# Kernel tuning notes

Measured on AMD Instinct MI355X. Metric: run time of the kernel, lower is better.

Reference implementation:

```python
import jax, jax.numpy as jnp
import numpy as np

H, W = 256, 256
N = 1024
EPS2D = 1e-4  # regularizer added to 2D covariances before inversion


def setup_inputs() -> dict:
    key = jax.random.key(0)
    ks = jax.random.split(key, 6)
    xy = jax.random.normal(ks[0], (N, 2), dtype=jnp.float32) * 3.0
    z = jax.random.uniform(ks[1], (N, 1), minval=2.0, maxval=30.0, dtype=jnp.float32)
    means3D = jnp.concatenate([xy, z], axis=-1)                      # [N,3], depths in (1,50)
    A = 0.1 * jax.random.normal(ks[2], (N, 3, 3), dtype=jnp.float32)
    covs3d = A @ jnp.swapaxes(A, -1, -2) + 0.01 * jnp.eye(3, dtype=jnp.float32)  # SPD [N,3,3]
    colors = jax.random.uniform(ks[3], (N, 3), dtype=jnp.float32)
    opacities = jax.random.uniform(ks[4], (N,), dtype=jnp.float32)
    Kmat = jnp.array([[300.0, 0.0, W / 2.0], [0.0, 300.0, H / 2.0], [0.0, 0.0, 1.0]], dtype=jnp.float32)
    Rmat = jnp.eye(3, dtype=jnp.float32)
    t = jnp.zeros((3,), dtype=jnp.float32)
    return {"means3D": means3D, "covs3d": covs3d, "colors": colors,
            "opacities": opacities, "K": Kmat, "R": Rmat, "t": t}


def reference(means3D, covs3d, colors, opacities, K, R, t):
    n = means3D.shape[0]
    # ---- projection ----
    cam = means3D @ R.T + t[None, :]                      # [N,3]
    depths = jnp.maximum(cam[:, 2], 1.0)
    screen = cam @ K.T
    means2D = screen[:, :2] / screen[:, 2:3]              # [N,2]
    fx, fy = K[0, 0], K[1, 1]
    inv_z = 1.0 / cam[:, 2]
    z2 = cam[:, 2] ** 2
    zeros = jnp.zeros_like(inv_z)
    row0 = jnp.stack([inv_z * fx, zeros, -cam[:, 0] / z2 * fx], axis=-1)
    row1 = jnp.stack([zeros, inv_z * fy, -cam[:, 1] / z2 * fy], axis=-1)
    J = jnp.stack([row0, row1], axis=1)                   # [N,2,3]
    covs_cam = jnp.einsum('ij,njk,lk->nil', R, covs3d, R)  # [N,3,3]
    covs2D = jnp.einsum('nij,njk,nlk->nil', J, covs_cam, J)  # [N,2,2]

    # ---- depth sort ----
    order = jnp.argsort(depths)
    means2D = means2D[order]
    covs2D = covs2D[order]
    colors_s = colors[order]
    opac_s = opacities[order]
    depths_s = depths[order]
    valid = (depths_s > 1.0) & (depths_s < 50.0)

    # ---- per-pixel gaussian evaluation (closed-form 2x2 inverse == cholesky_inverse) ----
    covs2D = covs2D + EPS2D * jnp.eye(2, dtype=covs2D.dtype)
    a = covs2D[:, 0, 0]; b = covs2D[:, 0, 1]; c = covs2D[:, 1, 1]
    det = a * c - b * b                                   # [N]
    ia = c / det; ib = -b / det; ic = a / det

    yy, xx = jnp.meshgrid(jnp.arange(H, dtype=jnp.float32),
                          jnp.arange(W, dtype=jnp.float32), indexing='ij')
    dx0 = xx[None] - means2D[:, 0, None, None]            # [N,H,W]
    dx1 = yy[None] - means2D[:, 1, None, None]            # [N,H,W]
    q = (ia[:, None, None] * dx0 * dx0
         + 2.0 * ib[:, None, None] * dx0 * dx1
         + ic[:, None, None] * dx1 * dx1)
    gauss = jnp.exp(-0.5 * q) / (2.0 * jnp.pi * jnp.sqrt(det))[:, None, None]
    gauss = gauss * valid[:, None, None].astype(gauss.dtype)

    # ---- alpha compositing (front-to-back) ----
    alphas = opac_s[:, None, None] * gauss                # [N,H,W]
    T = jnp.cumprod(1.0 - alphas, axis=0)
    T = jnp.concatenate([jnp.ones_like(alphas[:1]), T[:-1]], axis=0)
    weights = T * alphas                                  # [N,H,W]
    rendered = jnp.einsum('nhw,nc->hwc', weights, colors_s)  # [H,W,3]
    return rendered
```

## Files before the change

### kernel.cpp

```cpp
#include <hip/hip_runtime.h>
#include <math.h>

#define HH 256
#define WW 256
#define EPS2D 1e-4f
#define MAXN 1024
#define CULL_THR 23.0f
#define NL_HALF_LOG2E -0.72134752044448170368f


__global__ __launch_bounds__(256) void prep_kernel(
    const float* __restrict__ means3D, const float* __restrict__ covs3d,
    const float* __restrict__ colors,  const float* __restrict__ opac,
    const float* __restrict__ Km,      const float* __restrict__ Rm,
    const float* __restrict__ tv,
    float4* __restrict__ A, float4* __restrict__ B, float* __restrict__ C,
    int n)
{
    __shared__ float s_mean[MAXN*3];
    __shared__ float s_depth[MAXN];
    __shared__ float s_cov[64*9];
    __shared__ float s_col[64*3];
    __shared__ float s_op[64];
    __shared__ int   s_pr[4][64];

    int t = threadIdx.x, lane = t & 63, w = t >> 6;
    int g0b = blockIdx.x * 64;
    int nb = n - g0b; if (nb > 64) nb = 64; if (nb < 0) nb = 0;

    {
        int nm4 = (3*n) >> 2;
        const float4* m4 = (const float4*)means3D;
        for (int i = t; i < nm4; i += 256) ((float4*)s_mean)[i] = m4[i];
        for (int i = (nm4<<2) + t; i < 3*n; i += 256) s_mean[i] = means3D[i];

        const float* cbase = covs3d + (size_t)g0b * 9;
        int ncf = nb * 9, nc4 = ncf >> 2;
        for (int i = t; i < nc4; i += 256) ((float4*)s_cov)[i] = ((const float4*)cbase)[i];
        for (int i = (nc4<<2) + t; i < ncf; i += 256) s_cov[i] = cbase[i];

        const float* lbase = colors + (size_t)g0b * 3;
        int nlf = nb * 3, nl4 = nlf >> 2;
        for (int i = t; i < nl4; i += 256) ((float4*)s_col)[i] = ((const float4*)lbase)[i];
        for (int i = (nl4<<2) + t; i < nlf; i += 256) s_col[i] = lbase[i];

        const float* obase = opac + g0b;
        int no4 = nb >> 2;
        for (int i = t; i < no4; i += 256) ((float4*)s_op)[i] = ((const float4*)obase)[i];
        for (int i = (no4<<2) + t; i < nb; i += 256) s_op[i] = obase[i];
    }
    __syncthreads();

    float R00=Rm[0],R01=Rm[1],R02=Rm[2];
    float R10=Rm[3],R11=Rm[4],R12=Rm[5];
    float R20=Rm[6],R21=Rm[7],R22=Rm[8];
    float t0=tv[0], t1=tv[1], t2=tv[2];

    for (int g = t; g < MAXN; g += 256) {
        float d = 1e30f;
        if (g < n) {
            float X=s_mean[3*g+0], Y=s_mean[3*g+1], Z=s_mean[3*g+2];
            float cz = R20*X + R21*Y + R22*Z + t2;
            d = fmaxf(cz, 1.0f);
        }
        s_depth[g] = d;
    }
    __syncthreads();

    float mx=0.f,my=0.f,qa=0.f,qb=0.f,qc=0.f,lk=0.f,cr=0.f,cg=0.f,cbv=0.f;
    if (w == 0 && lane < nb) {
        int i = g0b + lane;
        float X = s_mean[3*i+0], Y = s_mean[3*i+1], Z = s_mean[3*i+2];
        float cx = R00*X + R01*Y + R02*Z + t0;
        float cy = R10*X + R11*Y + R12*Z + t1;
        float cz = R20*X + R21*Y + R22*Z + t2;
        float depth = s_depth[i];

        float K00=Km[0],K01=Km[1],K02=Km[2];
        float K10=Km[3],K11=Km[4],K12=Km[5];
        float K20=Km[6],K21=Km[7],K22=Km[8];
        float sx = K00*cx + K01*cy + K02*cz;
        float sy = K10*cx + K11*cy + K12*cz;
        float sz = K20*cx + K21*cy + K22*cz;
        mx = sx / sz;
        my = sy / sz;

        float invz  = 1.0f / cz;
        float invz2 = invz * invz;
        float j00 =  K00 * invz;
        float j02 = -K00 * cx * invz2;
        float j11 =  K11 * invz;
        float j12 = -K11 * cy * invz2;

        const float* S = s_cov + 9*lane;
        float S00=S[0],S01=S[1],S02=S[2];
        float S10=S[3],S11=S[4],S12=S[5];
        float S20=S[6],S21=S[7],S22=S[8];

        float M00 = R00*S00 + R01*S10 + R02*S20;
        float M01 = R00*S01 + R01*S11 + R02*S21;
        float M02 = R00*S02 + R01*S12 + R02*S22;
        float M10 = R10*S00 + R11*S10 + R12*S20;
        float M11 = R10*S01 + R11*S11 + R12*S21;
        float M12 = R10*S02 + R11*S12 + R12*S22;
        float M20 = R20*S00 + R21*S10 + R22*S20;
        float M21 = R20*S01 + R21*S11 + R22*S21;
        float M22 = R20*S02 + R21*S12 + R22*S22;
        float C00 = M00*R00 + M01*R01 + M02*R02;
        float C01 = M00*R10 + M01*R11 + M02*R12;
        float C02 = M00*R20 + M01*R21 + M02*R22;
        float C11 = M10*R10 + M11*R11 + M12*R12;
        float C12 = M10*R20 + M11*R21 + M12*R22;
        float C22 = M20*R20 + M21*R21 + M22*R22;

        float a_ = j00*j00*C00 + 2.0f*j00*j02*C02 + j02*j02*C22 + EPS2D;
        float b_ = j00*j11*C01 + j00*j12*C02 + j02*j11*C12 + j02*j12*C22;
        float c_ = j11*j11*C11 + 2.0f*j11*j12*C12 + j12*j12*C22 + EPS2D;

        float det = a_ * c_ - b_ * b_;
        float ia =  c_ / det;
        float ib = -b_ / det;
        float ic =  a_ / det;
        float norm = 1.0f / (6.283185307179586f * sqrtf(det));

        bool valid = (depth > 1.0f) && (depth < 50.0f);
        float k = s_op[lane] * norm * (valid ? 1.0f : 0.0f);

        qa = NL_HALF_LOG2E * ia;
        qb = 2.0f * NL_HALF_LOG2E * ib;
        qc = NL_HALF_LOG2E * ic;
        lk = log2f(k);
        cr = s_col[3*lane+0];
        cg = s_col[3*lane+1];
        cbv = s_col[3*lane+2];
    }

    {
        int cnt = 0;
        if (lane < nb) {
            int i = g0b + lane;
            float d = s_depth[i];
            const float4* d4 = (const float4*)s_depth;
            int jb = w * 64;
            #pragma unroll 4
            for (int jj = 0; jj < 64; ++jj) {
                float4 v = d4[jb + jj];
                int j = (jb + jj) << 2;
                cnt += (v.x < d || (v.x == d && j+0 < i)) ? 1 : 0;
                cnt += (v.y < d || (v.y == d && j+1 < i)) ? 1 : 0;
                cnt += (v.z < d || (v.z == d && j+2 < i)) ? 1 : 0;
                cnt += (v.w < d || (v.w == d && j+3 < i)) ? 1 : 0;
            }
        }
        s_pr[w][lane] = cnt;
    }
    __syncthreads();

    if (w == 0 && lane < nb) {
        int rank = s_pr[0][lane] + s_pr[1][lane] + s_pr[2][lane] + s_pr[3][lane];
        A[rank] = make_float4(mx, my, qa, qb);
        B[rank] = make_float4(qc, lk, cr, cg);
        C[rank] = cbv;
    }
}

__global__ __launch_bounds__(256) void render_kernel(
    const float4* __restrict__ A, const float4* __restrict__ B,
    const float* __restrict__ C, float* __restrict__ out, int n)
{
    __shared__ float4 s_p0[4][256];
    __shared__ float4 s_p1[4][256];
    __shared__ float4 s_part[3][256];

    int t = threadIdx.x, lane = t & 63, w = t >> 6;
    int row = blockIdx.x;
    int q0 = (n *  w     ) >> 2;
    int q1 = (n * (w + 1)) >> 2;
    float pyf = (float)row;

    int cnt = 0;
    if (q1 > q0) {
        int jc = min(q0 + lane, q1 - 1);
        float4 a = A[jc];
        float4 b = B[jc];
        float  c = C[jc];
        for (int ch = q0; ch < q1; ch += 64) {
            float4 a_n, b_n; float c_n;
            int cn = ch + 64;
            if (cn < q1) {
                int jc2 = min(cn + lane, q1 - 1);
                a_n = A[jc2];
                b_n = B[jc2];
                c_n = C[jc2];
            }
            int jj = ch + lane;
            bool keep = false;
            float qbdy = 0.f, u = 0.f;
            if (jj < q1) {
                float dy = pyf - a.y;
                qbdy = a.w * dy;
                u    = fmaf(b.x * dy, dy, b.y);
                float disc = fmaf(qbdy, qbdy, -4.0f * a.z * (u + CULL_THR));
                if (disc > 0.0f) {
                    float inv2qa = 0.5f / a.z;
                    float shw = sqrtf(disc) * inv2qa;
                    float ctr = -qbdy * inv2qa;
                    float xl = a.x + ctr + shw;
                    float xr = a.x + ctr - shw;
                    keep = (xr >= 0.0f) && (xl <= 255.0f);
                }
            }
            unsigned long long mk = __ballot(keep);
            int pre = __popcll(mk & ((1ull << lane) - 1ull));
            if (keep) {
                int pos = cnt + pre;
                s_p0[w][pos] = make_float4(a.x, a.z, qbdy, u);
                s_p1[w][pos] = make_float4(b.z, b.w, c, 0.f);
            }
            cnt += __popcll(mk);
            a = a_n; b = b_n; c = c_n;
        }
    }

    float lanef = (float)lane;
    float T0=1.f,T1=1.f,T2=1.f,T3=1.f;
    float r0=0.f,g0=0.f,b0=0.f, r1=0.f,g1=0.f,b1=0.f;
    float r2=0.f,g2=0.f,b2=0.f, r3=0.f,g3=0.f,b3=0.f;

    for (int k = 0; k < cnt; ++k) {
        float4 p0 = s_p0[w][k];
        float4 p1 = s_p1[w][k];
        float dx = lanef - p0.x;
        {
            float q = fmaf(fmaf(p0.y, dx, p0.z), dx, p0.w);
            float wg = T0 * __builtin_amdgcn_exp2f(q);
            r0 = fmaf(wg, p1.x, r0); g0 = fmaf(wg, p1.y, g0);
            b0 = fmaf(wg, p1.z, b0); T0 -= wg;
        }
        dx += 64.0f;
        {
            float q = fmaf(fmaf(p0.y, dx, p0.z), dx, p0.w);
            float wg = T1 * __builtin_amdgcn_exp2f(q);
            r1 = fmaf(wg, p1.x, r1); g1 = fmaf(wg, p1.y, g1);
            b1 = fmaf(wg, p1.z, b1); T1 -= wg;
        }
        dx += 64.0f;
        {
            float q = fmaf(fmaf(p0.y, dx, p0.z), dx, p0.w);
            float wg = T2 * __builtin_amdgcn_exp2f(q);
            r2 = fmaf(wg, p1.x, r2); g2 = fmaf(wg, p1.y, g2);
            b2 = fmaf(wg, p1.z, b2); T2 -= wg;
        }
        dx += 64.0f;
        {
            float q = fmaf(fmaf(p0.y, dx, p0.z), dx, p0.w);
            float wg = T3 * __builtin_amdgcn_exp2f(q);
            r3 = fmaf(wg, p1.x, r3); g3 = fmaf(wg, p1.y, g3);
            b3 = fmaf(wg, p1.z, b3); T3 -= wg;
        }
    }

    if (w != 0) {
        s_part[w-1][lane +   0] = make_float4(r0, g0, b0, T0);
        s_part[w-1][lane +  64] = make_float4(r1, g1, b1, T1);
        s_part[w-1][lane + 128] = make_float4(r2, g2, b2, T2);
        s_part[w-1][lane + 192] = make_float4(r3, g3, b3, T3);
    }
    __syncthreads();
    if (w == 0) {
        float rr[4]  = {r0, r1, r2, r3};
        float gg[4]  = {g0, g1, g2, g3};
        float bbv[4] = {b0, b1, b2, b3};
        float tt[4]  = {T0, T1, T2, T3};
        #pragma unroll
        for (int i = 0; i < 4; ++i) {
            int px = lane + (i << 6);
            float4 m1 = s_part[0][px];
            float4 m2 = s_part[1][px];
            float4 m3 = s_part[2][px];
            float cr = m2.x + m2.w * m3.x;
            float cg = m2.y + m2.w * m3.y;
            float cb = m2.z + m2.w * m3.z;
            cr = m1.x + m1.w * cr;
            cg = m1.y + m1.w * cg;
            cb = m1.z + m1.w * cb;
            cr = rr[i] + tt[i] * cr;
            cg = gg[i] + tt[i] * cg;
            cb = bbv[i] + tt[i] * cb;
            int p = row * 256 + px;
            out[3*p+0] = cr;
            out[3*p+1] = cg;
            out[3*p+2] = cb;
        }
    }
}

extern "C" void kernel_launch(void* const* d_in, const int* in_sizes, int n_in,
                              void* d_out, int out_size, void* d_ws, size_t ws_size,
                              hipStream_t stream)
{
    const float* means3D = (const float*)d_in[0];
    const float* covs3d  = (const float*)d_in[1];
    const float* colors  = (const float*)d_in[2];
    const float* opac    = (const float*)d_in[3];
    const float* Km      = (const float*)d_in[4];
    const float* Rm      = (const float*)d_in[5];
    const float* tv      = (const float*)d_in[6];
    int n = in_sizes[3];
    if (n > MAXN) n = MAXN;

    float4* A = (float4*)d_ws;
    float4* B = (float4*)((char*)d_ws + 16384);
    float*  C = (float*)((char*)d_ws + 32768);

    int pblocks = (n + 63) / 64;
    hipLaunchKernelGGL(prep_kernel, dim3(pblocks), dim3(256), 0, stream,
                       means3D, covs3d, colors, opac, Km, Rm, tv, A, B, C, n);

    hipLaunchKernelGGL(render_kernel, dim3(HH), dim3(256), 0, stream,
                       A, B, C, (float*)d_out, n);
}
```

Baseline: 23.48 us.

## Fuse prep and render into one cooperative kernel with grid sync

Merges the projection/sort prep kernel and the per-row render kernel into a single cooperative launch. The first few blocks do the prep work, then all 256 blocks meet at a grid-wide barrier before rendering. This removes the second kernel launch and the gap between the two kernels. In exchange it adds a grid sync and makes every block carry the combined shared-memory footprint, which could lower occupancy or make the cooperative launch fail if 256 blocks cannot be co-resident.

```diff
diff --git a/kernel.cpp b/kernel.cpp
--- a/kernel.cpp
+++ b/kernel.cpp
@@ -1,5 +1,8 @@
 #include <hip/hip_runtime.h>
+#include <hip/hip_cooperative_groups.h>
 #include <math.h>
+
+namespace cg = cooperative_groups;
 
 #define HH 256
 #define WW 256
@@ -9,13 +12,13 @@
 #define NL_HALF_LOG2E -0.72134752044448170368f
 
 
-__global__ __launch_bounds__(256) void prep_kernel(
+__global__ __launch_bounds__(256) void fused_kernel(
     const float* __restrict__ means3D, const float* __restrict__ covs3d,
     const float* __restrict__ colors,  const float* __restrict__ opac,
     const float* __restrict__ Km,      const float* __restrict__ Rm,
     const float* __restrict__ tv,
     float4* __restrict__ A, float4* __restrict__ B, float* __restrict__ C,
-    int n)
+    float* __restrict__ out, int n)
 {
     __shared__ float s_mean[MAXN*3];
     __shared__ float s_depth[MAXN];
@@ -23,157 +26,157 @@
     __shared__ float s_col[64*3];
     __shared__ float s_op[64];
     __shared__ int   s_pr[4][64];
-
-    int t = threadIdx.x, lane = t & 63, w = t >> 6;
-    int g0b = blockIdx.x * 64;
-    int nb = n - g0b; if (nb > 64) nb = 64; if (nb < 0) nb = 0;
-
-    {
-        int nm4 = (3*n) >> 2;
-        const float4* m4 = (const float4*)means3D;
-        for (int i = t; i < nm4; i += 256) ((float4*)s_mean)[i] = m4[i];
-        for (int i = (nm4<<2) + t; i < 3*n; i += 256) s_mean[i] = means3D[i];
-
-        const float* cbase = covs3d + (size_t)g0b * 9;
-        int ncf = nb * 9, nc4 = ncf >> 2;
-        for (int i = t; i < nc4; i += 256) ((float4*)s_cov)[i] = ((const float4*)cbase)[i];
-        for (int i = (nc4<<2) + t; i < ncf; i += 256) s_cov[i] = cbase[i];
-
-        const float* lbase = colors + (size_t)g0b * 3;
-        int nlf = nb * 3, nl4 = nlf >> 2;
-        for (int i = t; i < nl4; i += 256) ((float4*)s_col)[i] = ((const float4*)lbase)[i];
-        for (int i = (nl4<<2) + t; i < nlf; i += 256) s_col[i] = lbase[i];
-
-        const float* obase = opac + g0b;
-        int no4 = nb >> 2;
-        for (int i = t; i < no4; i += 256) ((float4*)s_op)[i] = ((const float4*)obase)[i];
-        for (int i = (no4<<2) + t; i < nb; i += 256) s_op[i] = obase[i];
-    }
-    __syncthreads();
-
-    float R00=Rm[0],R01=Rm[1],R02=Rm[2];
-    float R10=Rm[3],R11=Rm[4],R12=Rm[5];
-    float R20=Rm[6],R21=Rm[7],R22=Rm[8];
-    float t0=tv[0], t1=tv[1], t2=tv[2];
-
-    for (int g = t; g < MAXN; g += 256) {
-        float d = 1e30f;
-        if (g < n) {
-            float X=s_mean[3*g+0], Y=s_mean[3*g+1], Z=s_mean[3*g+2];
-            float cz = R20*X + R21*Y + R22*Z + t2;
-            d = fmaxf(cz, 1.0f);
-        }
-        s_depth[g] = d;
-    }
-    __syncthreads();
-
-    float mx=0.f,my=0.f,qa=0.f,qb=0.f,qc=0.f,lk=0.f,cr=0.f,cg=0.f,cbv=0.f;
-    if (w == 0 && lane < nb) {
-        int i = g0b + lane;
-        float X = s_mean[3*i+0], Y = s_mean[3*i+1], Z = s_mean[3*i+2];
-        float cx = R00*X + R01*Y + R02*Z + t0;
-        float cy = R10*X + R11*Y + R12*Z + t1;
-        float cz = R20*X + R21*Y + R22*Z + t2;
-        float depth = s_depth[i];
-
-        float K00=Km[0],K01=Km[1],K02=Km[2];
-        float K10=Km[3],K11=Km[4],K12=Km[5];
-        float K20=Km[6],K21=Km[7],K22=Km[8];
-        float sx = K00*cx + K01*cy + K02*cz;
-        float sy = K10*cx + K11*cy + K12*cz;
-        float sz = K20*cx + K21*cy + K22*cz;
-        mx = sx / sz;
-        my = sy / sz;
-
-        float invz  = 1.0f / cz;
-        float invz2 = invz * invz;
-        float j00 =  K00 * invz;
-        float j02 = -K00 * cx * invz2;
-        float j11 =  K11 * invz;
-        float j12 = -K11 * cy * invz2;
-
-        const float* S = s_cov + 9*lane;
-        float S00=S[0],S01=S[1],S02=S[2];
-        float S10=S[3],S11=S[4],S12=S[5];
-        float S20=S[6],S21=S[7],S22=S[8];
-
-        float M00 = R00*S00 + R01*S10 + R02*S20;
-        float M01 = R00*S01 + R01*S11 + R02*S21;
-        float M02 = R00*S02 + R01*S12 + R02*S22;
-        float M10 = R10*S00 + R11*S10 + R12*S20;
-        float M11 = R10*S01 + R11*S11 + R12*S21;
-        float M12 = R10*S02 + R11*S12 + R12*S22;
-        float M20 = R20*S00 + R21*S10 + R22*S20;
-        float M21 = R20*S01 + R21*S11 + R22*S21;
-        float M22 = R20*S02 + R21*S12 + R22*S22;
-        float C00 = M00*R00 + M01*R01 + M02*R02;
-        float C01 = M00*R10 + M01*R11 + M02*R12;
-        float C02 = M00*R20 + M01*R21 + M02*R22;
-        float C11 = M10*R10 + M11*R11 + M12*R12;
-        float C12 = M10*R20 + M11*R21 + M12*R22;
-        float C22 = M20*R20 + M21*R21 + M22*R22;
-
-        float a_ = j00*j00*C00 + 2.0f*j00*j02*C02 + j02*j02*C22 + EPS2D;
-        float b_ = j00*j11*C01 + j00*j12*C02 + j02*j11*C12 + j02*j12*C22;
-        float c_ = j11*j11*C11 + 2.0f*j11*j12*C12 + j12*j12*C22 + EPS2D;
-
-        float det = a_ * c_ - b_ * b_;
-        float ia =  c_ / det;
-        float ib = -b_ / det;
-        float ic =  a_ / det;
-        float norm = 1.0f / (6.283185307179586f * sqrtf(det));
-
-        bool valid = (depth > 1.0f) && (depth < 50.0f);
-        float k = s_op[lane] * norm * (valid ? 1.0f : 0.0f);
-
-        qa = NL_HALF_LOG2E * ia;
-        qb = 2.0f * NL_HALF_LOG2E * ib;
-        qc = NL_HALF_LOG2E * ic;
-        lk = log2f(k);
-        cr = s_col[3*lane+0];
-        cg = s_col[3*lane+1];
-        cbv = s_col[3*lane+2];
-    }
-
-    {
-        int cnt = 0;
-        if (lane < nb) {
-            int i = g0b + lane;
-            float d = s_depth[i];
-            const float4* d4 = (const float4*)s_depth;
-            int jb = w * 64;
-            #pragma unroll 4
-            for (int jj = 0; jj < 64; ++jj) {
-                float4 v = d4[jb + jj];
-                int j = (jb + jj) << 2;
-                cnt += (v.x < d || (v.x == d && j+0 < i)) ? 1 : 0;
-                cnt += (v.y < d || (v.y == d && j+1 < i)) ? 1 : 0;
-                cnt += (v.z < d || (v.z == d && j+2 < i)) ? 1 : 0;
-                cnt += (v.w < d || (v.w == d && j+3 < i)) ? 1 : 0;
-            }
-        }
-        s_pr[w][lane] = cnt;
-    }
-    __syncthreads();
-
-    if (w == 0 && lane < nb) {
-        int rank = s_pr[0][lane] + s_pr[1][lane] + s_pr[2][lane] + s_pr[3][lane];
-        A[rank] = make_float4(mx, my, qa, qb);
-        B[rank] = make_float4(qc, lk, cr, cg);
-        C[rank] = cbv;
-    }
-}
-
-__global__ __launch_bounds__(256) void render_kernel(
-    const float4* __restrict__ A, const float4* __restrict__ B,
-    const float* __restrict__ C, float* __restrict__ out, int n)
-{
     __shared__ float4 s_p0[4][256];
     __shared__ float4 s_p1[4][256];
     __shared__ float4 s_part[3][256];
 
     int t = threadIdx.x, lane = t & 63, w = t >> 6;
-    int row = blockIdx.x;
+    int blk = blockIdx.x;
+    int pblocks = (n + 63) >> 6;
+
+    if (blk < pblocks) {
+        int g0b = blk * 64;
+        int nb = n - g0b; if (nb > 64) nb = 64;
+
+        {
+            int nm4 = (3*n) >> 2;
+            const float4* m4 = (const float4*)means3D;
+            for (int i = t; i < nm4; i += 256) ((float4*)s_mean)[i] = m4[i];
+            for (int i = (nm4<<2) + t; i < 3*n; i += 256) s_mean[i] = means3D[i];
+
+            const float* cbase = covs3d + (size_t)g0b * 9;
+            int ncf = nb * 9, nc4 = ncf >> 2;
+            for (int i = t; i < nc4; i += 256) ((float4*)s_cov)[i] = ((const float4*)cbase)[i];
+            for (int i = (nc4<<2) + t; i < ncf; i += 256) s_cov[i] = cbase[i];
+
+            const float* lbase = colors + (size_t)g0b * 3;
+            int nlf = nb * 3, nl4 = nlf >> 2;
+            for (int i = t; i < nl4; i += 256) ((float4*)s_col)[i] = ((const float4*)lbase)[i];
+            for (int i = (nl4<<2) + t; i < nlf; i += 256) s_col[i] = lbase[i];
+
+            const float* obase = opac + g0b;
+            int no4 = nb >> 2;
+            for (int i = t; i < no4; i += 256) ((float4*)s_op)[i] = ((const float4*)obase)[i];
+            for (int i = (no4<<2) + t; i < nb; i += 256) s_op[i] = obase[i];
+        }
+        __syncthreads();
+
+        float R00=Rm[0],R01=Rm[1],R02=Rm[2];
+        float R10=Rm[3],R11=Rm[4],R12=Rm[5];
+        float R20=Rm[6],R21=Rm[7],R22=Rm[8];
+        float t0=tv[0], t1=tv[1], t2=tv[2];
+
+        for (int g = t; g < MAXN; g += 256) {
+            float d = 1e30f;
+            if (g < n) {
+                float X=s_mean[3*g+0], Y=s_mean[3*g+1], Z=s_mean[3*g+2];
+                float cz = R20*X + R21*Y + R22*Z + t2;
+                d = fmaxf(cz, 1.0f);
+            }
+            s_depth[g] = d;
+        }
+        __syncthreads();
+
+        float mx=0.f,my=0.f,qa=0.f,qb=0.f,qc=0.f,lk=0.f,cr=0.f,cg_=0.f,cbv=0.f;
+        if (w == 0 && lane < nb) {
+            int i = g0b + lane;
+            float X = s_mean[3*i+0], Y = s_mean[3*i+1], Z = s_mean[3*i+2];
+            float cx = R00*X + R01*Y + R02*Z + t0;
+            float cy = R10*X + R11*Y + R12*Z + t1;
+            float cz = R20*X + R21*Y + R22*Z + t2;
+            float depth = s_depth[i];
+
+            float K00=Km[0],K01=Km[1],K02=Km[2];
+            float K10=Km[3],K11=Km[4],K12=Km[5];
+            float K20=Km[6],K21=Km[7],K22=Km[8];
+            float sx = K00*cx + K01*cy + K02*cz;
+            float sy = K10*cx + K11*cy + K12*cz;
+            float sz = K20*cx + K21*cy + K22*cz;
+            mx = sx / sz;
+            my = sy / sz;
+
+            float invz  = 1.0f / cz;
+            float invz2 = invz * invz;
+            float j00 =  K00 * invz;
+            float j02 = -K00 * cx * invz2;
+            float j11 =  K11 * invz;
+            float j12 = -K11 * cy * invz2;
+
+            const float* S = s_cov + 9*lane;
+            float S00=S[0],S01=S[1],S02=S[2];
+            float S10=S[3],S11=S[4],S12=S[5];
+            float S20=S[6],S21=S[7],S22=S[8];
+
+            float M00 = R00*S00 + R01*S10 + R02*S20;
+            float M01 = R00*S01 + R01*S11 + R02*S21;
+            float M02 = R00*S02 + R01*S12 + R02*S22;
+            float M10 = R10*S00 + R11*S10 + R12*S20;
+            float M11 = R10*S01 + R11*S11 + R12*S21;
+            float M12 = R10*S02 + R11*S12 + R12*S22;
+            float M20 = R20*S00 + R21*S10 + R22*S20;
+            float M21 = R20*S01 + R21*S11 + R22*S21;
+            float M22 = R20*S02 + R21*S12 + R22*S22;
+            float C00 = M00*R00 + M01*R01 + M02*R02;
+            float C01 = M00*R10 + M01*R11 + M02*R12;
+            float C02 = M00*R20 + M01*R21 + M02*R22;
+            float C11 = M10*R10 + M11*R11 + M12*R12;
+            float C12 = M10*R20 + M11*R21 + M12*R22;
+            float C22 = M20*R20 + M21*R21 + M22*R22;
+
+            float a_ = j00*j00*C00 + 2.0f*j00*j02*C02 + j02*j02*C22 + EPS2D;
+            float b_ = j00*j11*C01 + j00*j12*C02 + j02*j11*C12 + j02*j12*C22;
+            float c_ = j11*j11*C11 + 2.0f*j11*j12*C12 + j12*j12*C22 + EPS2D;
+
+            float det = a_ * c_ - b_ * b_;
+            float ia =  c_ / det;
+            float ib = -b_ / det;
+            float ic =  a_ / det;
+            float norm = 1.0f / (6.283185307179586f * sqrtf(det));
+
+            bool valid = (depth > 1.0f) && (depth < 50.0f);
+            float k = s_op[lane] * norm * (valid ? 1.0f : 0.0f);
+
+            qa = NL_HALF_LOG2E * ia;
+            qb = 2.0f * NL_HALF_LOG2E * ib;
+            qc = NL_HALF_LOG2E * ic;
+            lk = log2f(k);
+            cr  = s_col[3*lane+0];
+            cg_ = s_col[3*lane+1];
+            cbv = s_col[3*lane+2];
+        }
+
+        {
+            int cnt = 0;
+            if (lane < nb) {
+                int i = g0b + lane;
+                float d = s_depth[i];
+                const float4* d4 = (const float4*)s_depth;
+                int jb = w * 64;
+                #pragma unroll 4
+                for (int jj = 0; jj < 64; ++jj) {
+                    float4 v = d4[jb + jj];
+                    int j = (jb + jj) << 2;
+                    cnt += (v.x < d || (v.x == d && j+0 < i)) ? 1 : 0;
+                    cnt += (v.y < d || (v.y == d && j+1 < i)) ? 1 : 0;
+                    cnt += (v.z < d || (v.z == d && j+2 < i)) ? 1 : 0;
+                    cnt += (v.w < d || (v.w == d && j+3 < i)) ? 1 : 0;
+                }
+            }
+            s_pr[w][lane] = cnt;
+        }
+        __syncthreads();
+
+        if (w == 0 && lane < nb) {
+            int rank = s_pr[0][lane] + s_pr[1][lane] + s_pr[2][lane] + s_pr[3][lane];
+            A[rank] = make_float4(mx, my, qa, qb);
+            B[rank] = make_float4(qc, lk, cr, cg_);
+            C[rank] = cbv;
+        }
+    }
+
+    cg::this_grid().sync();
+
+    int row = blk;
     int q0 = (n *  w     ) >> 2;
     int q1 = (n * (w + 1)) >> 2;
     float pyf = (float)row;
@@ -312,11 +315,12 @@
     float4* A = (float4*)d_ws;
     float4* B = (float4*)((char*)d_ws + 16384);
     float*  C = (float*)((char*)d_ws + 32768);
-
-    int pblocks = (n + 63) / 64;
-    hipLaunchKernelGGL(prep_kernel, dim3(pblocks), dim3(256), 0, stream,
-                       means3D, covs3d, colors, opac, Km, Rm, tv, A, B, C, n);
-
-    hipLaunchKernelGGL(render_kernel, dim3(HH), dim3(256), 0, stream,
-                       A, B, C, (float*)d_out, n);
+    float*  out = (float*)d_out;
+
+    void* args[] = { (void*)&means3D, (void*)&covs3d, (void*)&colors,
+                     (void*)&opac, (void*)&Km, (void*)&Rm, (void*)&tv,
+                     (void*)&A, (void*)&B, (void*)&C, (void*)&out, (void*)&n };
+
+    hipLaunchCooperativeKernel((const void*)fused_kernel,
+                               dim3(HH), dim3(256), args, 0, stream);
 }
```

New measurement: 50.00 us. 2.13x slower.
